# Optimization experiments

Hardware: AMD Instinct MI355X
Metric: run time of the kernel (lower is better)

The kernel has to match this reference:

```python
import jax, jax.numpy as jnp
import numpy as np

N_NODES = 50000
IN_CH = 128
HID = 32
HEADS = 4
OUT_CH = 32
N_EDGES = 1600000
NEG_SLOPE = 0.2


def _gatv2(x, src, dst, Wl, bl, Wr, br, att, bias, H, C):
    """GATv2Conv (PyG semantics, add_self_loops already applied to src/dst).
    x: [N, F_in]; src/dst: [E]; Wl/Wr: [F_in, H*C]; att: [H, C]; bias: [H*C].
    Returns [N, H*C] (concat heads)."""
    N = x.shape[0]
    xl = (x @ Wl + bl).reshape(N, H, C)  # source-side transform
    xr = (x @ Wr + br).reshape(N, H, C)  # target-side transform
    e = jax.nn.leaky_relu(xl[src] + xr[dst], NEG_SLOPE)  # [E, H, C]
    logits = jnp.einsum('ehc,hc->eh', e, att)  # [E, H]
    # softmax over incoming edges of each target node (stable)
    m = jax.ops.segment_max(logits, dst, num_segments=N)[dst]
    p = jnp.exp(logits - m)
    denom = jax.ops.segment_sum(p, dst, num_segments=N)[dst]
    alpha = p / denom  # [E, H]
    out = jax.ops.segment_sum(alpha[:, :, None] * xl[src], dst, num_segments=N)
    return out.reshape(N, H * C) + bias


def setup_inputs() -> dict:
    key = jax.random.key(0)
    ks = jax.random.split(key, 16)
    s1 = 1.0 / np.sqrt(IN_CH)
    s2 = 1.0 / np.sqrt(HID * HEADS)
    inp = {
        'x': jax.random.normal(ks[0], (N_NODES, IN_CH), jnp.float32),
        'edge_index': jax.random.randint(ks[1], (2, N_EDGES), 0, N_NODES, jnp.int64 if jax.config.read('jax_enable_x64') else jnp.int32).astype(jnp.int32),
        # layer 1: in -> HID per head, HEADS heads
        'Wl1': jax.random.normal(ks[2], (IN_CH, HEADS * HID), jnp.float32) * s1,
        'bl1': jnp.zeros((HEADS * HID,), jnp.float32),
        'Wr1': jax.random.normal(ks[3], (IN_CH, HEADS * HID), jnp.float32) * s1,
        'br1': jnp.zeros((HEADS * HID,), jnp.float32),
        'att1': jax.random.normal(ks[4], (HEADS, HID), jnp.float32) * s1,
        'b1': jnp.zeros((HEADS * HID,), jnp.float32),
        # mu head: HID*HEADS -> OUT_CH, 1 head
        'Wl_mu': jax.random.normal(ks[5], (HEADS * HID, OUT_CH), jnp.float32) * s2,
        'bl_mu': jnp.zeros((OUT_CH,), jnp.float32),
        'Wr_mu': jax.random.normal(ks[6], (HEADS * HID, OUT_CH), jnp.float32) * s2,
        'br_mu': jnp.zeros((OUT_CH,), jnp.float32),
        'att_mu': jax.random.normal(ks[7], (1, OUT_CH), jnp.float32) * s2,
        'b_mu': jnp.zeros((OUT_CH,), jnp.float32),
        # logvar head
        'Wl_lv': jax.random.normal(ks[8], (HEADS * HID, OUT_CH), jnp.float32) * s2,
        'bl_lv': jnp.zeros((OUT_CH,), jnp.float32),
        'Wr_lv': jax.random.normal(ks[9], (HEADS * HID, OUT_CH), jnp.float32) * s2,
        'br_lv': jnp.zeros((OUT_CH,), jnp.float32),
        'att_lv': jax.random.normal(ks[10], (1, OUT_CH), jnp.float32) * s2,
        'b_lv': jnp.zeros((OUT_CH,), jnp.float32),
    }
    return inp


def reference(x, edge_index, Wl1, bl1, Wr1, br1, att1, b1,
              Wl_mu, bl_mu, Wr_mu, br_mu, att_mu, b_mu,
              Wl_lv, bl_lv, Wr_lv, br_lv, att_lv, b_lv):
    N = x.shape[0]
    loops = jnp.arange(N, dtype=edge_index.dtype)
    src = jnp.concatenate([edge_index[0], loops])  # add_self_loops=True
    dst = jnp.concatenate([edge_index[1], loops])
    h = jax.nn.relu(_gatv2(x, src, dst, Wl1, bl1, Wr1, br1, att1, b1, HEADS, HID))
    mu = _gatv2(h, src, dst, Wl_mu, bl_mu, Wr_mu, br_mu, att_mu, b_mu, 1, OUT_CH)
    logvar = _gatv2(h, src, dst, Wl_lv, bl_lv, Wr_lv, br_lv, att_lv, b_lv, 1, OUT_CH)
    return (mu, logvar)
```

## Files before the change

### kernel.cpp

```cpp
#include <hip/hip_runtime.h>
#include <hip/hip_fp16.h>

#define NNODES 50000
#define EORIG  1600000
#define ETOT   (EORIG + NNODES)
#define NEG 0.2f
#define BSH 7
#define NBUCK ((NNODES + 127) >> BSH)
#define BCAP 5120
#define NRT (NNODES / 16)
#define EPB 4096
#define LOG2E 1.44269504f

typedef _Float16 v2h __attribute__((ext_vector_type(2)));
typedef _Float16 v8h __attribute__((ext_vector_type(8)));
typedef float    v4f __attribute__((ext_vector_type(4)));

__device__ __forceinline__ float hdot2v(v2h a, v2h b, float c) {
#if __has_builtin(__builtin_amdgcn_fdot2)
    return __builtin_amdgcn_fdot2(a, b, c, false);
#else
    return c + (float)a.x * (float)b.x + (float)a.y * (float)b.y;
#endif
}

__device__ __forceinline__ float fexp2(float t) {
#if __has_builtin(__builtin_amdgcn_exp2f)
    return __builtin_amdgcn_exp2f(t);
#else
    return exp2f(t);
#endif
}

__global__ __launch_bounds__(256) void wcvt_kernel(
    const float* __restrict__ Wl, const float* __restrict__ Wr,
    const float* __restrict__ Wlmu, const float* __restrict__ Wllv,
    const float* __restrict__ Wrmu, const float* __restrict__ Wrlv,
    __half* __restrict__ WT, __half* __restrict__ WT2, int* __restrict__ bcur)
{
    int id = blockIdx.x * 256 + threadIdx.x;
    if (id < NBUCK) bcur[id] = 0;
    if (id < 32768) {
        int k = id >> 8, c = id & 255;
        float v = (c < 128) ? Wl[k * 128 + c] : Wr[k * 128 + (c - 128)];
        WT[c * 128 + k] = __float2half(v);
    } else if (id < 49152) {
        int loc = id - 32768;
        int k = loc >> 7, c = loc & 127;
        int sel = c >> 5, cc = c & 31;
        const float* W = sel == 0 ? Wlmu : sel == 1 ? Wllv : sel == 2 ? Wrmu : Wrlv;
        WT2[c * 128 + k] = __float2half(W[k * 32 + cc]);
    }
}

__global__ __launch_bounds__(256) void lin1_kernel(
    const float* __restrict__ x, const __half* __restrict__ WT,
    const float* __restrict__ bl, const float* __restrict__ br,
    __half* __restrict__ xl16, __half* __restrict__ xr16)
{
    int rt = (blockIdx.x * 256 + threadIdx.x) >> 6;
    if (rt >= NRT) return;
    int l  = threadIdx.x & 63;
    int lr = l & 15, lg = l >> 4;
    int row = rt * 16 + lr;

    v8h a[4];
    const float4* xrow = reinterpret_cast<const float4*>(x + (size_t)row * 128);
    #pragma unroll
    for (int ks = 0; ks < 4; ++ks) {
        float4 f0 = xrow[ks * 8 + lg * 2];
        float4 f1 = xrow[ks * 8 + lg * 2 + 1];
        v8h t;
        t[0]=(_Float16)f0.x; t[1]=(_Float16)f0.y; t[2]=(_Float16)f0.z; t[3]=(_Float16)f0.w;
        t[4]=(_Float16)f1.x; t[5]=(_Float16)f1.y; t[6]=(_Float16)f1.z; t[7]=(_Float16)f1.w;
        a[ks] = t;
    }

    const uint4* wt4 = reinterpret_cast<const uint4*>(WT);
    #pragma unroll 4
    for (int ct = 0; ct < 16; ++ct) {
        int c = ct * 16 + lr;
        v4f acc = {0.f, 0.f, 0.f, 0.f};
        #pragma unroll
        for (int ks = 0; ks < 4; ++ks) {
            union { uint4 u; v8h h; } B;
            B.u = wt4[(size_t)c * 16 + ks * 4 + lg];
            acc = __builtin_amdgcn_mfma_f32_16x16x32_f16(a[ks], B.h, acc, 0, 0, 0);
        }
        float bb = (c < 128) ? bl[c] : br[c - 128];
        #pragma unroll
        for (int j = 0; j < 4; ++j) {
            int orow = rt * 16 + lg * 4 + j;
            __half hv = __float2half(acc[j] + bb);
            if (c < 128) xl16[(size_t)orow * 128 + c] = hv;
            else         xr16[(size_t)orow * 128 + (c - 128)] = hv;
        }
    }
}

__global__ __launch_bounds__(256) void lin2_kernel(
    const __half* __restrict__ h16, const __half* __restrict__ WT2,
    const float* __restrict__ blmu, const float* __restrict__ bllv,
    const float* __restrict__ brmu, const float* __restrict__ brlv,
    __half* __restrict__ xi16, __half* __restrict__ xrI16)
{
    int rt = (blockIdx.x * 256 + threadIdx.x) >> 6;
    if (rt >= NRT) return;
    int l  = threadIdx.x & 63;
    int lr = l & 15, lg = l >> 4;
    int row = rt * 16 + lr;

    v8h a[4];
    const uint4* hrow = reinterpret_cast<const uint4*>(h16 + (size_t)row * 128);
    #pragma unroll
    for (int ks = 0; ks < 4; ++ks) {
        union { uint4 u; v8h h; } A;
        A.u = hrow[ks * 4 + lg];
        a[ks] = A.h;
    }

    const uint4* wt4 = reinterpret_cast<const uint4*>(WT2);
    #pragma unroll 4
    for (int ct = 0; ct < 8; ++ct) {
        int c = ct * 16 + lr;
        v4f acc = {0.f, 0.f, 0.f, 0.f};
        #pragma unroll
        for (int ks = 0; ks < 4; ++ks) {
            union { uint4 u; v8h h; } B;
            B.u = wt4[(size_t)c * 16 + ks * 4 + lg];
            acc = __builtin_amdgcn_mfma_f32_16x16x32_f16(a[ks], B.h, acc, 0, 0, 0);
        }
        int sel = c >> 5, cc = c & 31;
        const float* bp = sel == 0 ? blmu : sel == 1 ? bllv : sel == 2 ? brmu : brlv;
        float bb = bp[cc];
        #pragma unroll
        for (int j = 0; j < 4; ++j) {
            int orow = rt * 16 + lg * 4 + j;
            __half hv = __float2half(acc[j] + bb);
            if (c < 64) xi16 [(size_t)orow * 64 + c]      = hv;
            else        xrI16[(size_t)orow * 64 + (c-64)] = hv;
        }
    }
}

__global__ __launch_bounds__(256) void part_kernel(
    const int* __restrict__ src, const int* __restrict__ dst,
    int* __restrict__ bcur, unsigned int* __restrict__ pairs)
{
    __shared__ int cnt[NBUCK];
    __shared__ int gbase[NBUCK];
    const int e0 = blockIdx.x * EPB;

    for (int i = threadIdx.x; i < NBUCK; i += 256) cnt[i] = 0;
    __syncthreads();

    for (int i = threadIdx.x; i < EPB; i += 256) {
        int e = e0 + i;
        if (e >= ETOT) break;
        int d = (e < EORIG) ? dst[e] : e - EORIG;
        atomicAdd(&cnt[d >> BSH], 1);
    }
    __syncthreads();

    for (int b = threadIdx.x; b < NBUCK; b += 256) {
        int c = cnt[b];
        gbase[b] = c ? (b * BCAP + atomicAdd(&bcur[b], c)) : 0;
        cnt[b] = 0;
    }
    __syncthreads();

    for (int i = threadIdx.x; i < EPB; i += 256) {
        int e = e0 + i;
        if (e >= ETOT) break;
        int s, d;
        if (e < EORIG) { s = src[e]; d = dst[e]; }
        else           { s = d = e - EORIG; }
        int b = d >> BSH;
        int slot = atomicAdd(&cnt[b], 1);
        pairs[gbase[b] + slot] = (unsigned)s | ((unsigned)(d & 127) << 16);
    }
}

__global__ __launch_bounds__(256) void csrfill_kernel(
    const unsigned int* __restrict__ pairs, const int* __restrict__ bcur,
    int2* __restrict__ begend, unsigned short* __restrict__ csr)
{
    __shared__ int cnt[128];
    __shared__ int lofs[128];
    __shared__ int scnt[128];
    const int b = blockIdx.x, n0 = b << BSH;
    const int nn = min(128, NNODES - n0);
    const int pbase = b * BCAP;
    const int pend = pbase + bcur[b];
    const int t = threadIdx.x;

    if (t < 128) { cnt[t] = 0; scnt[t] = 0; }
    __syncthreads();
    for (int i = pbase + t; i < pend; i += 256)
        atomicAdd(&cnt[pairs[i] >> 16], 1);
    __syncthreads();

    if (t < 128) lofs[t] = cnt[t];
    __syncthreads();
    for (int off = 1; off < 128; off <<= 1) {
        int v = (t < 128 && t >= off) ? lofs[t - off] : 0;
        __syncthreads();
        if (t < 128) lofs[t] += v;
        __syncthreads();
    }
    if (t < 128) lofs[t] = pbase + lofs[t] - cnt[t];
    __syncthreads();

    if (t < nn) begend[n0 + t] = make_int2(lofs[t], lofs[t] + cnt[t]);

    for (int i = pbase + t; i < pend; i += 256) {
        unsigned pr = pairs[i];
        int l = pr >> 16;
        int slot = atomicAdd(&scnt[l], 1);
        csr[lofs[l] + slot] = (unsigned short)(pr & 0xFFFFu);
    }
}

__global__ __launch_bounds__(256) void gat_gather1(
    const __half* __restrict__ xl16, const __half* __restrict__ xr16,
    const float* __restrict__ att, const float* __restrict__ bias,
    const int2* __restrict__ begend, const unsigned short* __restrict__ csr,
    __half* __restrict__ h16)
{
    int d = (blockIdx.x * 256 + threadIdx.x) >> 6;
    if (d >= NNODES) return;
    int lane = threadIdx.x & 63;
    int quarter = lane >> 4;
    int q = lane & 15;
    int qo = quarter * 4;

    v2h xrh[4], ath[4];
    {
        union { uint4 u; v2h v[4]; } R;
        R.u = reinterpret_cast<const uint4*>(xr16)[(size_t)d * 16 + q];
        #pragma unroll
        for (int j = 0; j < 4; ++j) xrh[j] = R.v[j];
        const float4* t4 = reinterpret_cast<const float4*>(att) + q * 2;
        float4 a = t4[0], b = t4[1];
        ath[0] = (v2h){(_Float16)(a.x*LOG2E), (_Float16)(a.y*LOG2E)};
        ath[1] = (v2h){(_Float16)(a.z*LOG2E), (_Float16)(a.w*LOG2E)};
        ath[2] = (v2h){(_Float16)(b.x*LOG2E), (_Float16)(b.y*LOG2E)};
        ath[3] = (v2h){(_Float16)(b.z*LOG2E), (_Float16)(b.w*LOG2E)};
    }
    const v2h neg2 = (v2h){(_Float16)NEG, (_Float16)NEG};

    int2 be = begend[d];
    int beg = be.x, end = be.y;
    int nI = (end - beg + 15) >> 4;
    const uint4* xlu = reinterpret_cast<const uint4*>(xl16);

    float den = 0.f;
    float acc[8] = {0.f,0.f,0.f,0.f,0.f,0.f,0.f,0.f};

    auto compute = [&](uint4 U, bool val) {
        union { uint4 u; v2h v[4]; } X; X.u = U;
        float t = 0.f;
        #pragma unroll
        for (int j = 0; j < 4; ++j) {
            v2h s = X.v[j] + xrh[j];
            v2h l = __builtin_elementwise_max(s, s * neg2);
            t = hdot2v(l, ath[j], t);
        }
        t += __shfl_xor(t, 1, 64);
        t += __shfl_xor(t, 2, 64);
        float p = val ? fexp2(t) : 0.f;
        den += p;
        #pragma unroll
        for (int j = 0; j < 4; ++j) {
            acc[2*j]   += p * (float)X.v[j].x;
            acc[2*j+1] += p * (float)X.v[j].y;
        }
    };

    int  iA[4], iB[4];
    bool vA[4], vB[4];
    uint4 rA[4];

    #pragma unroll
    for (int k = 0; k < 4; ++k) {
        int s = beg + qo + k;
        vA[k] = s < end;
        iA[k] = csr[vA[k] ? s : end - 1];
    }
    #pragma unroll
    for (int k = 0; k < 4; ++k) rA[k] = xlu[(size_t)iA[k] * 16 + q];
    #pragma unroll
    for (int k = 0; k < 4; ++k) {
        int s = beg + 16 + qo + k;
        vB[k] = s < end;
        iB[k] = csr[vB[k] ? s : end - 1];
    }

    for (int it = 0; it < nI; ++it) {
        int b2 = beg + (it + 2) * 16;
        int  iC[4]; bool vC[4];
        #pragma unroll
        for (int k = 0; k < 4; ++k) {
            int s = b2 + qo + k;
            vC[k] = s < end;
            iC[k] = csr[vC[k] ? s : end - 1];
        }
        uint4 rB[4];
        #pragma unroll
        for (int k = 0; k < 4; ++k) rB[k] = xlu[(size_t)iB[k] * 16 + q];
        #pragma unroll
        for (int k = 0; k < 4; ++k) compute(rA[k], vA[k]);
        #pragma unroll
        for (int k = 0; k < 4; ++k) {
            rA[k] = rB[k]; vA[k] = vB[k];
            iB[k] = iC[k]; vB[k] = vC[k];
        }
    }

    den += __shfl_xor(den, 16, 64);
    den += __shfl_xor(den, 32, 64);
    #pragma unroll
    for (int j = 0; j < 8; ++j) {
        acc[j] += __shfl_xor(acc[j], 16, 64);
        acc[j] += __shfl_xor(acc[j], 32, 64);
    }

    if (quarter == 0) {
        float r = 1.f / den;
        const float4* bp = reinterpret_cast<const float4*>(bias) + q * 2;
        float4 ba = bp[0], bb = bp[1];
        __half hv[8];
        hv[0] = __float2half(fmaxf(acc[0]*r+ba.x, 0.f));
        hv[1] = __float2half(fmaxf(acc[1]*r+ba.y, 0.f));
        hv[2] = __float2half(fmaxf(acc[2]*r+ba.z, 0.f));
        hv[3] = __float2half(fmaxf(acc[3]*r+ba.w, 0.f));
        hv[4] = __float2half(fmaxf(acc[4]*r+bb.x, 0.f));
        hv[5] = __float2half(fmaxf(acc[5]*r+bb.y, 0.f));
        hv[6] = __float2half(fmaxf(acc[6]*r+bb.z, 0.f));
        hv[7] = __float2half(fmaxf(acc[7]*r+bb.w, 0.f));
        *reinterpret_cast<uint4*>(&h16[(size_t)d * 128 + q * 8]) =
            *reinterpret_cast<uint4*>(hv);
    }
}

__global__ __launch_bounds__(256) void gat_gather2(
    const __half* __restrict__ xi16, const __half* __restrict__ xrI16,
    const float* __restrict__ atmu, const float* __restrict__ atlv,
    const float* __restrict__ bmu,  const float* __restrict__ blv,
    const int2* __restrict__ begend, const unsigned short* __restrict__ csr,
    float* __restrict__ out)
{
    int d = (blockIdx.x * 256 + threadIdx.x) >> 6;
    if (d >= NNODES) return;
    int lane = threadIdx.x & 63;
    int oct = lane >> 3;
    int r   = lane & 7;
    bool lv = r >= 4;
    int cq  = lv ? r - 4 : r;
    int oo = oct * 2;

    v2h xrh[4], ath[4];
    {
        union { uint4 u; v2h v[4]; } R;
        R.u = reinterpret_cast<const uint4*>(xrI16)[(size_t)d * 8 + r];
        #pragma unroll
        for (int j = 0; j < 4; ++j) xrh[j] = R.v[j];
        const float4* t4 = reinterpret_cast<const float4*>(lv ? atlv : atmu) + cq * 2;
        float4 a = t4[0], b = t4[1];
        ath[0] = (v2h){(_Float16)(a.x*LOG2E), (_Float16)(a.y*LOG2E)};
        ath[1] = (v2h){(_Float16)(a.z*LOG2E), (_Float16)(a.w*LOG2E)};
        ath[2] = (v2h){(_Float16)(b.x*LOG2E), (_Float16)(b.y*LOG2E)};
        ath[3] = (v2h){(_Float16)(b.z*LOG2E), (_Float16)(b.w*LOG2E)};
    }
    const v2h neg2 = (v2h){(_Float16)NEG, (_Float16)NEG};

    int2 be = begend[d];
    int beg = be.x, end = be.y;
    int nI = (end - beg + 15) >> 4;
    const uint4* xiu = reinterpret_cast<const uint4*>(xi16);

    float den = 0.f;
    float acc[8] = {0.f,0.f,0.f,0.f,0.f,0.f,0.f,0.f};

    auto compute = [&](uint4 U, bool val) {
        union { uint4 u; v2h v[4]; } X; X.u = U;
        float t = 0.f;
        #pragma unroll
        for (int j = 0; j < 4; ++j) {
            v2h s = X.v[j] + xrh[j];
            v2h l = __builtin_elementwise_max(s, s * neg2);
            t = hdot2v(l, ath[j], t);
        }
        t += __shfl_xor(t, 1, 64);
        t += __shfl_xor(t, 2, 64);
        float p = val ? fexp2(t) : 0.f;
        den += p;
        #pragma unroll
        for (int j = 0; j < 4; ++j) {
            acc[2*j]   += p * (float)X.v[j].x;
            acc[2*j+1] += p * (float)X.v[j].y;
        }
    };

    int  iA[2], iB[2];
    bool vA[2], vB[2];
    uint4 rA[2];

    #pragma unroll
    for (int k = 0; k < 2; ++k) {
        int s = beg + oo + k;
        vA[k] = s < end;
        iA[k] = csr[vA[k] ? s : end - 1];
    }
    #pragma unroll
    for (int k = 0; k < 2; ++k) rA[k] = xiu[(size_t)iA[k] * 8 + r];
    #pragma unroll
    for (int k = 0; k < 2; ++k) {
        int s = beg + 16 + oo + k;
        vB[k] = s < end;
        iB[k] = csr[vB[k] ? s : end - 1];
    }

    for (int it = 0; it < nI; ++it) {
        int b2 = beg + (it + 2) * 16;
        int  iC[2]; bool vC[2];
        #pragma unroll
        for (int k = 0; k < 2; ++k) {
            int s = b2 + oo + k;
            vC[k] = s < end;
            iC[k] = csr[vC[k] ? s : end - 1];
        }
        uint4 rB[2];
        #pragma unroll
        for (int k = 0; k < 2; ++k) rB[k] = xiu[(size_t)iB[k] * 8 + r];
        #pragma unroll
        for (int k = 0; k < 2; ++k) compute(rA[k], vA[k]);
        #pragma unroll
        for (int k = 0; k < 2; ++k) {
            rA[k] = rB[k]; vA[k] = vB[k];
            iB[k] = iC[k]; vB[k] = vC[k];
        }
    }

    den += __shfl_xor(den, 8, 64);
    den += __shfl_xor(den, 16, 64);
    den += __shfl_xor(den, 32, 64);
    #pragma unroll
    for (int j = 0; j < 8; ++j) {
        acc[j] += __shfl_xor(acc[j], 8, 64);
        acc[j] += __shfl_xor(acc[j], 16, 64);
        acc[j] += __shfl_xor(acc[j], 32, 64);
    }

    if (oct == 0) {
        float rr = 1.f / den;
        const float4* bp = reinterpret_cast<const float4*>(lv ? blv : bmu) + cq * 2;
        float4 ba = bp[0], bb = bp[1];
        float4 o1 = make_float4(acc[0]*rr+ba.x, acc[1]*rr+ba.y,
                                acc[2]*rr+ba.z, acc[3]*rr+ba.w);
        float4 o2 = make_float4(acc[4]*rr+bb.x, acc[5]*rr+bb.y,
                                acc[6]*rr+bb.z, acc[7]*rr+bb.w);
        float* base_out = out + (lv ? 1600000 : 0);
        float4* op = reinterpret_cast<float4*>(base_out) + (size_t)d * 8 + cq * 2;
        op[0] = o1; op[1] = o2;
    }
}

extern "C" void kernel_launch(void* const* d_in, const int* in_sizes, int n_in,
                              void* d_out, int out_size, void* d_ws, size_t ws_size,
                              hipStream_t stream) {
    const float* x    = (const float*)d_in[0];
    const int*   ei   = (const int*)d_in[1];
    const float* Wl1  = (const float*)d_in[2];
    const float* bl1  = (const float*)d_in[3];
    const float* Wr1  = (const float*)d_in[4];
    const float* br1  = (const float*)d_in[5];
    const float* att1 = (const float*)d_in[6];
    const float* b1   = (const float*)d_in[7];
    const float* Wlmu = (const float*)d_in[8];
    const float* blmu = (const float*)d_in[9];
    const float* Wrmu = (const float*)d_in[10];
    const float* brmu = (const float*)d_in[11];
    const float* atmu = (const float*)d_in[12];
    const float* bmu  = (const float*)d_in[13];
    const float* Wllv = (const float*)d_in[14];
    const float* bllv = (const float*)d_in[15];
    const float* Wrlv = (const float*)d_in[16];
    const float* brlv = (const float*)d_in[17];
    const float* atlv = (const float*)d_in[18];
    const float* blv  = (const float*)d_in[19];

    float* out = (float*)d_out;
    float* ws  = (float*)d_ws;

    __half* xl16 = (__half*)ws;
    __half* xr16 = (__half*)(ws + 3200000);
    __half* h16  = (__half*)(ws + 6400000);
    __half* WT   = (__half*)(ws + 9600000);
    __half* WT2  = (__half*)(ws + 9620000);

    __half* xi16  = (__half*)ws;
    __half* xrI16 = (__half*)(ws + 1600000);

    int* ip = (int*)(ws + 10000000);
    unsigned int*   pairs  = (unsigned int*)ip;
    int*            bcur   = ip + 2001920;
    int2*           begend = (int2*)(ip + 2002312);
    unsigned short* csr    = (unsigned short*)(ip + 2102312);

    const int* srcp = ei;
    const int* dstp = ei + EORIG;

    const int NBE = (ETOT + EPB - 1) / EPB;

    wcvt_kernel<<<192, 256, 0, stream>>>(Wl1, Wr1, Wlmu, Wllv, Wrmu, Wrlv, WT, WT2, bcur);

    part_kernel<<<NBE, 256, 0, stream>>>(srcp, dstp, bcur, pairs);
    csrfill_kernel<<<NBUCK, 256, 0, stream>>>(pairs, bcur, begend, csr);

    lin1_kernel<<<(NRT + 3) / 4, 256, 0, stream>>>(x, WT, bl1, br1, xl16, xr16);

    gat_gather1<<<(NNODES * 64 + 255) / 256, 256, 0, stream>>>(
        xl16, xr16, att1, b1, begend, csr, h16);

    lin2_kernel<<<(NRT + 3) / 4, 256, 0, stream>>>(
        h16, WT2, blmu, bllv, brmu, brlv, xi16, xrI16);

    gat_gather2<<<(NNODES * 64 + 255) / 256, 256, 0, stream>>>(
        xi16, xrI16, atmu, atlv, bmu, blv, begend, csr, out);
}
```

Before: 198.5 us.

## Merge weight conversion into partition kernel and regranularize gather loops to eight edges

Weight transposition and conversion now run as extra blocks of the edge-partition kernel, and the bucket counter is zeroed by an async memset, so there is one fewer kernel launch. Both GAT gather kernels now step through edges eight per iteration: full iterations run without masking, and a single masked pass handles the remaining edges. This cuts wasted lanes and predication on low-degree nodes, and 64-bit index math is replaced with 32-bit. The trade-off is fewer outstanding gathers per lane in the first-layer gather. Prefetches also read CSR entries past each node's range without bounds checks.

```diff
diff --git a/kernel.cpp b/kernel.cpp
--- a/kernel.cpp
+++ b/kernel.cpp
@@ -10,6 +10,7 @@
 #define BCAP 5120
 #define NRT (NNODES / 16)
 #define EPB 4096
+#define NBE ((ETOT + EPB - 1) / EPB)
 #define LOG2E 1.44269504f
 
 typedef _Float16 v2h __attribute__((ext_vector_type(2)));
@@ -32,121 +33,30 @@
 #endif
 }
 
-__global__ __launch_bounds__(256) void wcvt_kernel(
+__global__ __launch_bounds__(256) void prep_kernel(
+    const int* __restrict__ src, const int* __restrict__ dst,
+    int* __restrict__ bcur, unsigned int* __restrict__ pairs,
     const float* __restrict__ Wl, const float* __restrict__ Wr,
     const float* __restrict__ Wlmu, const float* __restrict__ Wllv,
     const float* __restrict__ Wrmu, const float* __restrict__ Wrlv,
-    __half* __restrict__ WT, __half* __restrict__ WT2, int* __restrict__ bcur)
+    __half* __restrict__ WT, __half* __restrict__ WT2)
 {
-    int id = blockIdx.x * 256 + threadIdx.x;
-    if (id < NBUCK) bcur[id] = 0;
-    if (id < 32768) {
-        int k = id >> 8, c = id & 255;
-        float v = (c < 128) ? Wl[k * 128 + c] : Wr[k * 128 + (c - 128)];
-        WT[c * 128 + k] = __float2half(v);
-    } else if (id < 49152) {
-        int loc = id - 32768;
-        int k = loc >> 7, c = loc & 127;
-        int sel = c >> 5, cc = c & 31;
-        const float* W = sel == 0 ? Wlmu : sel == 1 ? Wllv : sel == 2 ? Wrmu : Wrlv;
-        WT2[c * 128 + k] = __float2half(W[k * 32 + cc]);
-    }
-}
-
-__global__ __launch_bounds__(256) void lin1_kernel(
-    const float* __restrict__ x, const __half* __restrict__ WT,
-    const float* __restrict__ bl, const float* __restrict__ br,
-    __half* __restrict__ xl16, __half* __restrict__ xr16)
-{
-    int rt = (blockIdx.x * 256 + threadIdx.x) >> 6;
-    if (rt >= NRT) return;
-    int l  = threadIdx.x & 63;
-    int lr = l & 15, lg = l >> 4;
-    int row = rt * 16 + lr;
-
-    v8h a[4];
-    const float4* xrow = reinterpret_cast<const float4*>(x + (size_t)row * 128);
-    #pragma unroll
-    for (int ks = 0; ks < 4; ++ks) {
-        float4 f0 = xrow[ks * 8 + lg * 2];
-        float4 f1 = xrow[ks * 8 + lg * 2 + 1];
-        v8h t;
-        t[0]=(_Float16)f0.x; t[1]=(_Float16)f0.y; t[2]=(_Float16)f0.z; t[3]=(_Float16)f0.w;
-        t[4]=(_Float16)f1.x; t[5]=(_Float16)f1.y; t[6]=(_Float16)f1.z; t[7]=(_Float16)f1.w;
-        a[ks] = t;
-    }
-
-    const uint4* wt4 = reinterpret_cast<const uint4*>(WT);
-    #pragma unroll 4
-    for (int ct = 0; ct < 16; ++ct) {
-        int c = ct * 16 + lr;
-        v4f acc = {0.f, 0.f, 0.f, 0.f};
-        #pragma unroll
-        for (int ks = 0; ks < 4; ++ks) {
-            union { uint4 u; v8h h; } B;
-            B.u = wt4[(size_t)c * 16 + ks * 4 + lg];
-            acc = __builtin_amdgcn_mfma_f32_16x16x32_f16(a[ks], B.h, acc, 0, 0, 0);
-        }
-        float bb = (c < 128) ? bl[c] : br[c - 128];
-        #pragma unroll
-        for (int j = 0; j < 4; ++j) {
-            int orow = rt * 16 + lg * 4 + j;
-            __half hv = __float2half(acc[j] + bb);
-            if (c < 128) xl16[(size_t)orow * 128 + c] = hv;
-            else         xr16[(size_t)orow * 128 + (c - 128)] = hv;
-        }
-    }
-}
-
-__global__ __launch_bounds__(256) void lin2_kernel(
-    const __half* __restrict__ h16, const __half* __restrict__ WT2,
-    const float* __restrict__ blmu, const float* __restrict__ bllv,
-    const float* __restrict__ brmu, const float* __restrict__ brlv,
-    __half* __restrict__ xi16, __half* __restrict__ xrI16)
-{
-    int rt = (blockIdx.x * 256 + threadIdx.x) >> 6;
-    if (rt >= NRT) return;
-    int l  = threadIdx.x & 63;
-    int lr = l & 15, lg = l >> 4;
-    int row = rt * 16 + lr;
-
-    v8h a[4];
-    const uint4* hrow = reinterpret_cast<const uint4*>(h16 + (size_t)row * 128);
-    #pragma unroll
-    for (int ks = 0; ks < 4; ++ks) {
-        union { uint4 u; v8h h; } A;
-        A.u = hrow[ks * 4 + lg];
-        a[ks] = A.h;
-    }
-
-    const uint4* wt4 = reinterpret_cast<const uint4*>(WT2);
-    #pragma unroll 4
-    for (int ct = 0; ct < 8; ++ct) {
-        int c = ct * 16 + lr;
-        v4f acc = {0.f, 0.f, 0.f, 0.f};
-        #pragma unroll
-        for (int ks = 0; ks < 4; ++ks) {
-            union { uint4 u; v8h h; } B;
-            B.u = wt4[(size_t)c * 16 + ks * 4 + lg];
-            acc = __builtin_amdgcn_mfma_f32_16x16x32_f16(a[ks], B.h, acc, 0, 0, 0);
-        }
-        int sel = c >> 5, cc = c & 31;
-        const float* bp = sel == 0 ? blmu : sel == 1 ? bllv : sel == 2 ? brmu : brlv;
-        float bb = bp[cc];
-        #pragma unroll
-        for (int j = 0; j < 4; ++j) {
-            int orow = rt * 16 + lg * 4 + j;
-            __half hv = __float2half(acc[j] + bb);
-            if (c < 64) xi16 [(size_t)orow * 64 + c]      = hv;
-            else        xrI16[(size_t)orow * 64 + (c-64)] = hv;
-        }
-    }
-}
-
-__global__ __launch_bounds__(256) void part_kernel(
-    const int* __restrict__ src, const int* __restrict__ dst,
-    int* __restrict__ bcur, unsigned int* __restrict__ pairs)
-{
+    if (blockIdx.x >= NBE) {
+        int id = (blockIdx.x - NBE) * 256 + threadIdx.x;
+        if (id < 32768) {
+            int k = id >> 8, c = id & 255;
+            float v = (c < 128) ? Wl[k * 128 + c] : Wr[k * 128 + (c - 128)];
+            WT[c * 128 + k] = __float2half(v);
+        } else if (id < 49152) {
+            int loc = id - 32768;
+            int k = loc >> 7, c = loc & 127;
+            int sel = c >> 5, cc = c & 31;
+            const float* W = sel == 0 ? Wlmu : sel == 1 ? Wllv : sel == 2 ? Wrmu : Wrlv;
+            WT2[c * 128 + k] = __float2half(W[k * 32 + cc]);
+        }
+        return;
+    }
+
     __shared__ int cnt[NBUCK];
     __shared__ int gbase[NBUCK];
     const int e0 = blockIdx.x * EPB;
@@ -200,7 +110,8 @@
         atomicAdd(&cnt[pairs[i] >> 16], 1);
     __syncthreads();
 
-    if (t < 128) lofs[t] = cnt[t];
+    int myc = (t < 128) ? cnt[t] : 0;
+    if (t < 128) lofs[t] = myc;
     __syncthreads();
     for (int off = 1; off < 128; off <<= 1) {
         int v = (t < 128 && t >= off) ? lofs[t - off] : 0;
@@ -208,16 +119,106 @@
         if (t < 128) lofs[t] += v;
         __syncthreads();
     }
-    if (t < 128) lofs[t] = pbase + lofs[t] - cnt[t];
-    __syncthreads();
-
-    if (t < nn) begend[n0 + t] = make_int2(lofs[t], lofs[t] + cnt[t]);
+    if (t < 128) lofs[t] = pbase + lofs[t] - myc;
+    __syncthreads();
+
+    if (t < nn) begend[n0 + t] = make_int2(lofs[t], lofs[t] + myc);
 
     for (int i = pbase + t; i < pend; i += 256) {
         unsigned pr = pairs[i];
         int l = pr >> 16;
         int slot = atomicAdd(&scnt[l], 1);
         csr[lofs[l] + slot] = (unsigned short)(pr & 0xFFFFu);
+    }
+}
+
+__global__ __launch_bounds__(256) void lin1_kernel(
+    const float* __restrict__ x, const __half* __restrict__ WT,
+    const float* __restrict__ bl, const float* __restrict__ br,
+    __half* __restrict__ xl16, __half* __restrict__ xr16)
+{
+    int rt = (blockIdx.x * 256 + threadIdx.x) >> 6;
+    if (rt >= NRT) return;
+    int l  = threadIdx.x & 63;
+    int lr = l & 15, lg = l >> 4;
+    int row = rt * 16 + lr;
+
+    v8h a[4];
+    const float4* xrow = reinterpret_cast<const float4*>(x + (size_t)row * 128);
+    #pragma unroll
+    for (int ks = 0; ks < 4; ++ks) {
+        float4 f0 = xrow[ks * 8 + lg * 2];
+        float4 f1 = xrow[ks * 8 + lg * 2 + 1];
+        v8h t;
+        t[0]=(_Float16)f0.x; t[1]=(_Float16)f0.y; t[2]=(_Float16)f0.z; t[3]=(_Float16)f0.w;
+        t[4]=(_Float16)f1.x; t[5]=(_Float16)f1.y; t[6]=(_Float16)f1.z; t[7]=(_Float16)f1.w;
+        a[ks] = t;
+    }
+
+    const uint4* wt4 = reinterpret_cast<const uint4*>(WT);
+    #pragma unroll 4
+    for (int ct = 0; ct < 16; ++ct) {
+        int c = ct * 16 + lr;
+        v4f acc = {0.f, 0.f, 0.f, 0.f};
+        #pragma unroll
+        for (int ks = 0; ks < 4; ++ks) {
+            union { uint4 u; v8h h; } B;
+            B.u = wt4[(size_t)c * 16 + ks * 4 + lg];
+            acc = __builtin_amdgcn_mfma_f32_16x16x32_f16(a[ks], B.h, acc, 0, 0, 0);
+        }
+        float bb = (c < 128) ? bl[c] : br[c - 128];
+        #pragma unroll
+        for (int j = 0; j < 4; ++j) {
+            int orow = rt * 16 + lg * 4 + j;
+            __half hv = __float2half(acc[j] + bb);
+            if (c < 128) xl16[(size_t)orow * 128 + c] = hv;
+            else         xr16[(size_t)orow * 128 + (c - 128)] = hv;
+        }
+    }
+}
+
+__global__ __launch_bounds__(256) void lin2_kernel(
+    const __half* __restrict__ h16, const __half* __restrict__ WT2,
+    const float* __restrict__ blmu, const float* __restrict__ bllv,
+    const float* __restrict__ brmu, const float* __restrict__ brlv,
+    __half* __restrict__ xi16, __half* __restrict__ xrI16)
+{
+    int rt = (blockIdx.x * 256 + threadIdx.x) >> 6;
+    if (rt >= NRT) return;
+    int l  = threadIdx.x & 63;
+    int lr = l & 15, lg = l >> 4;
+    int row = rt * 16 + lr;
+
+    v8h a[4];
+    const uint4* hrow = reinterpret_cast<const uint4*>(h16 + (size_t)row * 128);
+    #pragma unroll
+    for (int ks = 0; ks < 4; ++ks) {
+        union { uint4 u; v8h h; } A;
+        A.u = hrow[ks * 4 + lg];
+        a[ks] = A.h;
+    }
+
+    const uint4* wt4 = reinterpret_cast<const uint4*>(WT2);
+    #pragma unroll 4
+    for (int ct = 0; ct < 8; ++ct) {
+        int c = ct * 16 + lr;
+        v4f acc = {0.f, 0.f, 0.f, 0.f};
+        #pragma unroll
+        for (int ks = 0; ks < 4; ++ks) {
+            union { uint4 u; v8h h; } B;
+            B.u = wt4[(size_t)c * 16 + ks * 4 + lg];
+            acc = __builtin_amdgcn_mfma_f32_16x16x32_f16(a[ks], B.h, acc, 0, 0, 0);
+        }
+        int sel = c >> 5, cc = c & 31;
+        const float* bp = sel == 0 ? blmu : sel == 1 ? bllv : sel == 2 ? brmu : brlv;
+        float bb = bp[cc];
+        #pragma unroll
+        for (int j = 0; j < 4; ++j) {
+            int orow = rt * 16 + lg * 4 + j;
+            __half hv = __float2half(acc[j] + bb);
+            if (c < 64) xi16 [(size_t)orow * 64 + c]      = hv;
+            else        xrI16[(size_t)orow * 64 + (c-64)] = hv;
+        }
     }
 }
 
@@ -232,12 +233,12 @@
     int lane = threadIdx.x & 63;
     int quarter = lane >> 4;
     int q = lane & 15;
-    int qo = quarter * 4;
+    int qo = quarter * 2;
 
     v2h xrh[4], ath[4];
     {
         union { uint4 u; v2h v[4]; } R;
-        R.u = reinterpret_cast<const uint4*>(xr16)[(size_t)d * 16 + q];
+        R.u = reinterpret_cast<const uint4*>(xr16)[d * 16 + q];
         #pragma unroll
         for (int j = 0; j < 4; ++j) xrh[j] = R.v[j];
         const float4* t4 = reinterpret_cast<const float4*>(att) + q * 2;
@@ -251,13 +252,34 @@
 
     int2 be = begend[d];
     int beg = be.x, end = be.y;
-    int nI = (end - beg + 15) >> 4;
+    int deg = end - beg;
+    int nF = deg >> 3;
+    int rem = deg & 7;
     const uint4* xlu = reinterpret_cast<const uint4*>(xl16);
 
     float den = 0.f;
     float acc[8] = {0.f,0.f,0.f,0.f,0.f,0.f,0.f,0.f};
 
-    auto compute = [&](uint4 U, bool val) {
+    auto computeU = [&](uint4 U) {
+        union { uint4 u; v2h v[4]; } X; X.u = U;
+        float t = 0.f;
+        #pragma unroll
+        for (int j = 0; j < 4; ++j) {
+            v2h s = X.v[j] + xrh[j];
+            v2h l = __builtin_elementwise_max(s, s * neg2);
+            t = hdot2v(l, ath[j], t);
+        }
+        t += __shfl_xor(t, 1, 64);
+        t += __shfl_xor(t, 2, 64);
+        float p = fexp2(t);
+        den += p;
+        #pragma unroll
+        for (int j = 0; j < 4; ++j) {
+            acc[2*j]   += p * (float)X.v[j].x;
+            acc[2*j+1] += p * (float)X.v[j].y;
+        }
+    };
+    auto computeM = [&](uint4 U, bool val) {
         union { uint4 u; v2h v[4]; } X; X.u = U;
         float t = 0.f;
         #pragma unroll
@@ -277,44 +299,23 @@
         }
     };
 
-    int  iA[4], iB[4];
-    bool vA[4], vB[4];
-    uint4 rA[4];
-
-    #pragma unroll
-    for (int k = 0; k < 4; ++k) {
-        int s = beg + qo + k;
-        vA[k] = s < end;
-        iA[k] = csr[vA[k] ? s : end - 1];
-    }
-    #pragma unroll
-    for (int k = 0; k < 4; ++k) rA[k] = xlu[(size_t)iA[k] * 16 + q];
-    #pragma unroll
-    for (int k = 0; k < 4; ++k) {
-        int s = beg + 16 + qo + k;
-        vB[k] = s < end;
-        iB[k] = csr[vB[k] ? s : end - 1];
-    }
-
-    for (int it = 0; it < nI; ++it) {
-        int b2 = beg + (it + 2) * 16;
-        int  iC[4]; bool vC[4];
-        #pragma unroll
-        for (int k = 0; k < 4; ++k) {
-            int s = b2 + qo + k;
-            vC[k] = s < end;
-            iC[k] = csr[vC[k] ? s : end - 1];
-        }
-        uint4 rB[4];
-        #pragma unroll
-        for (int k = 0; k < 4; ++k) rB[k] = xlu[(size_t)iB[k] * 16 + q];
-        #pragma unroll
-        for (int k = 0; k < 4; ++k) compute(rA[k], vA[k]);
-        #pragma unroll
-        for (int k = 0; k < 4; ++k) {
-            rA[k] = rB[k]; vA[k] = vB[k];
-            iB[k] = iC[k]; vB[k] = vC[k];
-        }
+    int iA0 = csr[beg + qo],     iA1 = csr[beg + qo + 1];
+    uint4 rA0 = xlu[iA0 * 16 + q], rA1 = xlu[iA1 * 16 + q];
+    int iB0 = csr[beg + 8 + qo], iB1 = csr[beg + 8 + qo + 1];
+
+    for (int it = 0; it < nF; ++it) {
+        int b2 = beg + (it + 2) * 8;
+        int iC0 = csr[b2 + qo], iC1 = csr[b2 + qo + 1];
+        uint4 rB0 = xlu[iB0 * 16 + q];
+        uint4 rB1 = xlu[iB1 * 16 + q];
+        computeU(rA0);
+        computeU(rA1);
+        rA0 = rB0; rA1 = rB1;
+        iB0 = iC0; iB1 = iC1;
+    }
+    if (rem) {
+        computeM(rA0, qo < rem);
+        computeM(rA1, qo + 1 < rem);
     }
 
     den += __shfl_xor(den, 16, 64);
@@ -357,12 +358,11 @@
     int r   = lane & 7;
     bool lv = r >= 4;
     int cq  = lv ? r - 4 : r;
-    int oo = oct * 2;
 
     v2h xrh[4], ath[4];
     {
         union { uint4 u; v2h v[4]; } R;
-        R.u = reinterpret_cast<const uint4*>(xrI16)[(size_t)d * 8 + r];
+        R.u = reinterpret_cast<const uint4*>(xrI16)[d * 8 + r];
         #pragma unroll
         for (int j = 0; j < 4; ++j) xrh[j] = R.v[j];
         const float4* t4 = reinterpret_cast<const float4*>(lv ? atlv : atmu) + cq * 2;
@@ -376,13 +376,34 @@
 
     int2 be = begend[d];
     int beg = be.x, end = be.y;
-    int nI = (end - beg + 15) >> 4;
+    int deg = end - beg;
+    int nF = deg >> 3;
+    int rem = deg & 7;
     const uint4* xiu = reinterpret_cast<const uint4*>(xi16);
 
     float den = 0.f;
     float acc[8] = {0.f,0.f,0.f,0.f,0.f,0.f,0.f,0.f};
 
-    auto compute = [&](uint4 U, bool val) {
+    auto computeU = [&](uint4 U) {
+        union { uint4 u; v2h v[4]; } X; X.u = U;
+        float t = 0.f;
+        #pragma unroll
+        for (int j = 0; j < 4; ++j) {
+            v2h s = X.v[j] + xrh[j];
+            v2h l = __builtin_elementwise_max(s, s * neg2);
+            t = hdot2v(l, ath[j], t);
+        }
+        t += __shfl_xor(t, 1, 64);
+        t += __shfl_xor(t, 2, 64);
+        float p = fexp2(t);
+        den += p;
+        #pragma unroll
+        for (int j = 0; j < 4; ++j) {
+            acc[2*j]   += p * (float)X.v[j].x;
+            acc[2*j+1] += p * (float)X.v[j].y;
+        }
+    };
+    auto computeM = [&](uint4 U, bool val) {
         union { uint4 u; v2h v[4]; } X; X.u = U;
         float t = 0.f;
         #pragma unroll
@@ -402,45 +423,17 @@
         }
     };
 
-    int  iA[2], iB[2];
-    bool vA[2], vB[2];
-    uint4 rA[2];
-
-    #pragma unroll
-    for (int k = 0; k < 2; ++k) {
-        int s = beg + oo + k;
-        vA[k] = s < end;
-        iA[k] = csr[vA[k] ? s : end - 1];
-    }
-    #pragma unroll
-    for (int k = 0; k < 2; ++k) rA[k] = xiu[(size_t)iA[k] * 8 + r];
-    #pragma unroll
-    for (int k = 0; k < 2; ++k) {
-        int s = beg + 16 + oo + k;
-        vB[k] = s < end;
-        iB[k] = csr[vB[k] ? s : end - 1];
-    }
-
-    for (int it = 0; it < nI; ++it) {
-        int b2 = beg + (it + 2) * 16;
-        int  iC[2]; bool vC[2];
-        #pragma unroll
-        for (int k = 0; k < 2; ++k) {
-            int s = b2 + oo + k;
-            vC[k] = s < end;
-            iC[k] = csr[vC[k] ? s : end - 1];
-        }
-        uint4 rB[2];
-        #pragma unroll
-        for (int k = 0; k < 2; ++k) rB[k] = xiu[(size_t)iB[k] * 8 + r];
-        #pragma unroll
-        for (int k = 0; k < 2; ++k) compute(rA[k], vA[k]);
-        #pragma unroll
-        for (int k = 0; k < 2; ++k) {
-            rA[k] = rB[k]; vA[k] = vB[k];
-            iB[k] = iC[k]; vB[k] = vC[k];
-        }
-    }
+    int iA = csr[beg + oct];
+    uint4 rA = xiu[iA * 8 + r];
+    int iB = csr[beg + 8 + oct];
+
+    for (int it = 0; it < nF; ++it) {
+        int iC = csr[beg + (it + 2) * 8 + oct];
+        uint4 rB = xiu[iB * 8 + r];
+        computeU(rA);
+        rA = rB; iB = iC;
+    }
+    if (rem) computeM(rA, oct < rem);
 
     den += __shfl_xor(den, 8, 64);
     den += __shfl_xor(den, 16, 64);
@@ -511,11 +504,9 @@
     const int* srcp = ei;
     const int* dstp = ei + EORIG;
 
-    const int NBE = (ETOT + EPB - 1) / EPB;
-
-    wcvt_kernel<<<192, 256, 0, stream>>>(Wl1, Wr1, Wlmu, Wllv, Wrmu, Wrlv, WT, WT2, bcur);
-
-    part_kernel<<<NBE, 256, 0, stream>>>(srcp, dstp, bcur, pairs);
+    hipMemsetAsync(bcur, 0, NBUCK * sizeof(int), stream);
+    prep_kernel<<<NBE + 192, 256, 0, stream>>>(
+        srcp, dstp, bcur, pairs, Wl1, Wr1, Wlmu, Wllv, Wrmu, Wrlv, WT, WT2);
     csrfill_kernel<<<NBUCK, 256, 0, stream>>>(pairs, bcur, begend, csr);
 
     lin1_kernel<<<(NRT + 3) / 4, 256, 0, stream>>>(x, WT, bl1, br1, xl16, xr16);
```

Result: no change. 199.7 us (+0.6%).
